# Kernel tuning notes

Hardware: AMD Instinct MI355X
Metric: run time of the kernel (lower is better)

## Reference

```python
import jax, jax.numpy as jnp
import numpy as np

B, SEQ, S, DIM_IN, DIM_K, DIM_V = 4, 2048, 128, 512, 64, 64
L = SEQ + 2 * S
NEG = -1e30  # stand-in for log(0) in the tril mask (finite for stable vjp)


def _layernorm(x, g, b, eps=1e-5):
    m = jnp.mean(x, axis=-1, keepdims=True)
    v = jnp.var(x, axis=-1, keepdims=True)
    return (x - m) / jnp.sqrt(v + eps) * g + b


def setup_inputs() -> dict:
    key = jax.random.key(0)
    ks = jax.random.split(key, 18)
    w = lambda k, shape, s=0.02: (jax.random.normal(k, shape, jnp.float32) * s)
    inp = {
        "x": jax.random.normal(ks[0], (B, L, DIM_IN), jnp.float32),
        "Wq": w(ks[1], (DIM_IN, DIM_K)),
        "Wk": w(ks[2], (DIM_IN, DIM_K)),
        "Wv": w(ks[3], (DIM_IN, DIM_V)),
        "Wq_s": w(ks[4], (DIM_IN, DIM_K)),
        "Wk_s": w(ks[5], (DIM_IN, DIM_K)),
        "Wv_s": w(ks[6], (DIM_IN, DIM_V)),
        "Wq_e": w(ks[7], (DIM_IN, DIM_K)),
        "Wk_e": w(ks[8], (DIM_IN, DIM_K)),
        "Wv_e": w(ks[9], (DIM_IN, DIM_V)),
        "ln_g": jnp.ones((DIM_IN,), jnp.float32),
        "ln_b": jnp.zeros((DIM_IN,), jnp.float32),
        "ln_s_g": jnp.ones((DIM_IN,), jnp.float32),
        "ln_s_b": jnp.zeros((DIM_IN,), jnp.float32),
        "ln_e_g": jnp.ones((DIM_IN,), jnp.float32),
        "ln_e_b": jnp.zeros((DIM_IN,), jnp.float32),
        "cope_emb": jax.random.normal(ks[10], (DIM_K, S), jnp.float32),
        "offset": 0,
    }
    return inp


def reference(x, Wq, Wk, Wv, Wq_s, Wk_s, Wv_s, Wq_e, Wk_e, Wv_e,
              ln_g, ln_b, ln_s_g, ln_s_b, ln_e_g, ln_e_b, cope_emb, offset):
    # extract_state: first/last state_len tokens
    xs, xm, xe = x[:, :S], x[:, S:L - S], x[:, -S:]
    xm = _layernorm(xm, ln_g, ln_b)
    xs = _layernorm(xs, ln_s_g, ln_s_b)
    xe = _layernorm(xe, ln_e_g, ln_e_b)

    q, k, v = xm @ Wq, xm @ Wk, xm @ Wv          # (B, SEQ, dk/dv)
    q_s, k_s, v_s = xs @ Wq_s, xs @ Wk_s, xs @ Wv_s
    q_e, k_e, v_e = xe @ Wq_e, xe @ Wk_e, xe @ Wv_e

    # CoPE bias over the non-state block
    logits = jnp.einsum('bqd,bkd->bqk', q, k)    # (B, SEQ, SEQ)
    gates = jax.nn.sigmoid(logits)
    pos = jnp.flip(jnp.cumsum(jnp.flip(gates, -1), axis=-1), -1)
    pos = jnp.minimum(pos, jnp.float32(S - 1))
    pos_ceil = jnp.ceil(pos).astype(jnp.int32)
    pos_floor = jnp.floor(pos).astype(jnp.int32)
    logits_int = jnp.einsum('bqd,dk->bqk', q, cope_emb)  # (B, SEQ, S)
    logits_c = jnp.take_along_axis(logits_int, pos_ceil, axis=-1)
    logits_f = jnp.take_along_axis(logits_int, pos_floor, axis=-1)
    wfrac = pos - pos_floor.astype(pos.dtype)
    bias = logits_c * wfrac + logits_f * (1.0 - wfrac)   # (B, SEQ, SEQ)

    q_full = jnp.concatenate([q_s, q, q_e], axis=1)      # (B, L, dk)
    k_full = jnp.concatenate([k_s, k, k_e], axis=1)
    v_full = jnp.concatenate([v_s, v, v_e], axis=1)

    # explicit tril log-mask bias with CoPE injected in the middle block
    tri = jnp.tril(jnp.ones((L, L), dtype=bool))
    attn_bias = jnp.where(tri, 0.0, NEG).astype(jnp.float32)
    attn_bias = jnp.broadcast_to(attn_bias, (B, L, L))
    attn_bias = attn_bias.at[:, S:L - S, S:L - S].add(bias)

    scale = 1.0 / jnp.sqrt(jnp.float32(DIM_K))
    scores = jnp.einsum('bqd,bkd->bqk', q_full, k_full) * scale + attn_bias
    att = jax.nn.softmax(scores, axis=-1)
    return jnp.einsum('bqk,bkd->bqd', att, v_full)       # (B, L, dv)
```

## Files before the change

kernel.cpp:

```cpp
#include <hip/hip_runtime.h>
#include <math.h>

#define B_    4
#define SEQ_  2048
#define S_    128
#define L_    2304
#define DIN   512
#define DK    64
#define NEGINF (-1e30f)
#define SCALE 0.125f
#define NCOLS 2176
#define NMID  8192
#define NEDGE 1024
#define LE    2304

typedef _Float16 f16;
typedef __attribute__((ext_vector_type(8))) _Float16 half8;
typedef __attribute__((ext_vector_type(4))) float f32x4;

union U4 { uint4 u; f16 h[8]; };

__global__ __launch_bounds__(256) void k_wsplit(
    const float* __restrict__ Wq,  const float* __restrict__ Wk,  const float* __restrict__ Wv,
    const float* __restrict__ Wqs, const float* __restrict__ Wks, const float* __restrict__ Wvs,
    const float* __restrict__ Wqe, const float* __restrict__ Wke, const float* __restrict__ Wve,
    const float* __restrict__ cope,
    f16* __restrict__ Wsp, f16* __restrict__ copesp)
{
    __shared__ float xs[64 * 68];
    const int kt  = blockIdx.x;
    const int mat = blockIdx.y;
    const int tid = threadIdx.x;

    if (mat == 9) {
        if (kt != 0) return;
        for (int half = 0; half < 2; ++half) {
            #pragma unroll
            for (int i = 0; i < 4; ++i) {
                int g = tid + 256 * i;
                int d = g >> 4, p4 = g & 15;
                *(float4*)(xs + d * 68 + p4 * 4) =
                    *(const float4*)(cope + (size_t)d * 128 + half * 64 + p4 * 4);
            }
            __syncthreads();
            if (tid < 128) {
                int pp = tid & 63, hf = tid >> 6;
                int d0 = hf * 32;
                for (int j = 0; j < 32; ++j) {
                    float v = xs[(d0 + j) * 68 + pp];
                    f16 hi = (f16)v;
                    copesp[(size_t)(half * 64 + pp) * 128 + d0 + j]      = hi;
                    copesp[(size_t)(half * 64 + pp) * 128 + 64 + d0 + j] = (f16)(v - (float)hi);
                }
            }
            __syncthreads();
        }
        return;
    }

    const float* W;
    switch (mat) {
        case 0: W = Wq;  break; case 1: W = Wk;  break; case 2: W = Wv;  break;
        case 3: W = Wqs; break; case 4: W = Wks; break; case 5: W = Wvs; break;
        case 6: W = Wqe; break; case 7: W = Wke; break; default: W = Wve; break;
    }
    const int k0  = kt * 64;
    #pragma unroll
    for (int i = 0; i < 4; ++i) {
        int g = tid + 256 * i;
        int k = g >> 4, c4 = g & 15;
        *(float4*)(xs + k * 68 + c4 * 4) = ((const float4*)W)[(size_t)(k0 + k) * 16 + c4];
    }
    __syncthreads();
    const int col = tid & 63, hf = tid >> 6;
    const int kk0 = hf * 16;
    U4 hi0, hi1, lo0, lo1;
    #pragma unroll
    for (int j = 0; j < 8; ++j) {
        float v0 = xs[(kk0 + j) * 68 + col];
        float v1 = xs[(kk0 + 8 + j) * 68 + col];
        hi0.h[j] = (f16)v0; lo0.h[j] = (f16)(v0 - (float)hi0.h[j]);
        hi1.h[j] = (f16)v1; lo1.h[j] = (f16)(v1 - (float)hi1.h[j]);
    }
    f16* dst = Wsp + (size_t)mat * 65536 + (size_t)col * 1024 + k0 + kk0;
    *(uint4*)(dst)       = hi0.u;
    *(uint4*)(dst + 8)   = hi1.u;
    *(uint4*)(dst + 512) = lo0.u;
    *(uint4*)(dst + 520) = lo1.u;
}

__global__ __launch_bounds__(256) void k_proj(
    const float* __restrict__ x, const f16* __restrict__ Wsp,
    const float* __restrict__ g0, const float* __restrict__ b0,
    const float* __restrict__ gs, const float* __restrict__ bs,
    const float* __restrict__ ge, const float* __restrict__ be,
    f16* __restrict__ qsp, f16* __restrict__ ksp, f16* __restrict__ vhT)
{
    __shared__ f16 As[32 * 136];
    __shared__ f16 Bs[3 * 64 * 136];
    __shared__ float mean_s[32], rstd_s[32];
    const int tid  = threadIdx.x;
    const int row0 = blockIdx.x * 32;
    const int rseq = row0 % L_;
    const int seg  = (rseq < S_) ? 0 : (rseq >= L_ - S_) ? 2 : 1;
    const int mat0 = (seg == 0) ? 3 : (seg == 2) ? 6 : 0;
    const float* gg = (seg == 0) ? gs : (seg == 2) ? ge : g0;
    const float* bb = (seg == 0) ? bs : (seg == 2) ? be : b0;

    {
        const int rr = tid >> 3, qq = tid & 7;
        const float4* xr = (const float4*)(x + (size_t)(row0 + rr) * DIN) + qq * 16;
        float s = 0.f, s2 = 0.f;
        #pragma unroll
        for (int i = 0; i < 16; ++i) {
            float4 v = xr[i];
            s  += v.x + v.y + v.z + v.w;
            s2 += v.x * v.x + v.y * v.y + v.z * v.z + v.w * v.w;
        }
        s  += __shfl_xor(s, 1);  s  += __shfl_xor(s, 2);  s  += __shfl_xor(s, 4);
        s2 += __shfl_xor(s2, 1); s2 += __shfl_xor(s2, 2); s2 += __shfl_xor(s2, 4);
        if (qq == 0) {
            float mean = s * (1.f / DIN);
            mean_s[rr] = mean;
            rstd_s[rr] = rsqrtf(s2 * (1.f / DIN) - mean * mean + 1e-5f);
        }
    }

    const int w = tid >> 6, lane = tid & 63;
    const int cl = lane & 15, quad = lane >> 4;
    const int r0 = 16 * (w >> 1), c0 = 32 * (w & 1);

    f32x4 acc[3][2];
    #pragma unroll
    for (int m = 0; m < 3; ++m)
        #pragma unroll
        for (int j = 0; j < 2; ++j) acc[m][j] = 0.f;

    for (int kc = 0; kc < DIN; kc += 64) {
        __syncthreads();
        {
            int r = tid >> 3, c8 = tid & 7;
            const float* xp = x + (size_t)(row0 + r) * DIN + kc + c8 * 8;
            float4 a0 = *(const float4*)xp;
            float4 a1 = *(const float4*)(xp + 4);
            float4 gA = *(const float4*)(gg + kc + c8 * 8);
            float4 gB = *(const float4*)(gg + kc + c8 * 8 + 4);
            float4 bA = *(const float4*)(bb + kc + c8 * 8);
            float4 bB = *(const float4*)(bb + kc + c8 * 8 + 4);
            float mean = mean_s[r], rstd = rstd_s[r];
            float n[8];
            n[0] = (a0.x - mean) * rstd * gA.x + bA.x;
            n[1] = (a0.y - mean) * rstd * gA.y + bA.y;
            n[2] = (a0.z - mean) * rstd * gA.z + bA.z;
            n[3] = (a0.w - mean) * rstd * gA.w + bA.w;
            n[4] = (a1.x - mean) * rstd * gB.x + bB.x;
            n[5] = (a1.y - mean) * rstd * gB.y + bB.y;
            n[6] = (a1.z - mean) * rstd * gB.z + bB.z;
            n[7] = (a1.w - mean) * rstd * gB.w + bB.w;
            U4 hi, lo;
            #pragma unroll
            for (int j = 0; j < 8; ++j) {
                hi.h[j] = (f16)n[j];
                lo.h[j] = (f16)(n[j] - (float)hi.h[j]);
            }
            *(uint4*)(As + r * 136 + c8 * 8)      = hi.u;
            *(uint4*)(As + r * 136 + 64 + c8 * 8) = lo.u;
        }
        #pragma unroll
        for (int i = 0; i < 6; ++i) {
            int g = tid + 256 * i;
            int mm = g >> 9, rem = g & 511;
            int col = rem >> 3, c8 = rem & 7;
            const f16* src = Wsp + (size_t)(mat0 + mm) * 65536 + (size_t)col * 1024 + kc + c8 * 8;
            f16* dst = Bs + mm * 8704 + col * 136 + c8 * 8;
            *(uint4*)(dst)      = *(const uint4*)(src);
            *(uint4*)(dst + 64) = *(const uint4*)(src + 512);
        }
        __syncthreads();
        #pragma unroll
        for (int h = 0; h < 2; ++h) {
            half8 ah, al;
            {
                const f16* base = As + (r0 + cl) * 136 + h * 32 + quad * 8;
                ah = *(const half8*)(base);
                al = *(const half8*)(base + 64);
            }
            #pragma unroll
            for (int m = 0; m < 3; ++m)
                #pragma unroll
                for (int cs = 0; cs < 2; ++cs) {
                    const f16* base = Bs + m * 8704 + (c0 + 16 * cs + cl) * 136 + h * 32 + quad * 8;
                    half8 bh = *(const half8*)(base);
                    half8 bl = *(const half8*)(base + 64);
                    acc[m][cs] = __builtin_amdgcn_mfma_f32_16x16x32_f16(ah, bh, acc[m][cs], 0, 0, 0);
                    acc[m][cs] = __builtin_amdgcn_mfma_f32_16x16x32_f16(ah, bl, acc[m][cs], 0, 0, 0);
                    acc[m][cs] = __builtin_amdgcn_mfma_f32_16x16x32_f16(al, bh, acc[m][cs], 0, 0, 0);
                }
        }
    }

    const int bI = row0 / L_;
    const int rb = row0 - bI * L_;
    #pragma unroll
    for (int m = 0; m < 3; ++m) {
        f16* sp = (m == 0) ? qsp : ksp;
        #pragma unroll
        for (int cs = 0; cs < 2; ++cs)
            #pragma unroll
            for (int r = 0; r < 4; ++r) {
                int lrow = r0 + quad * 4 + r;
                int col  = c0 + 16 * cs + cl;
                float v  = acc[m][cs][r];
                size_t grow = (size_t)(row0 + lrow);
                if (m < 2) {
                    f16 hv = (f16)v;
                    sp[grow * 128 + col]      = hv;
                    sp[grow * 128 + 64 + col] = (f16)(v - (float)hv);
                } else {
                    vhT[(size_t)(bI * 64 + col) * L_ + rb + lrow] = (f16)v;
                }
            }
    }
}

__global__ __launch_bounds__(512) void k_fmid(
    const f16* __restrict__ qsp, const f16* __restrict__ ksp,
    const f16* __restrict__ vhT, const f16* __restrict__ copesp,
    float* __restrict__ out)
{
    __shared__ f16 Qs[32 * 136];
    __shared__ f16 Ks[128 * 136];
    __shared__ f16 Vt[64 * 136];
    __shared__ float li[32 * 132];
    __shared__ float Tq[4][32], Tm[4][32], Ll[4][32];
    f16* const Ps = Ks + 64 * 136;

    const int tid = threadIdx.x;
    const int blk = blockIdx.x;
    const int b = blk >> 6, strip = blk & 63;
    const int q0 = strip * 32;
    const size_t rowbase = (size_t)b * L_ + S_ + q0;
    const int w = tid >> 6, lane = tid & 63;
    const int cl = lane & 15, quad = lane >> 4;
    const int g = w >> 2, ch = w & 3;
    const int tmax = ((q0 + 31) >> 7) + 1;

    {
        int r = tid >> 4, c = tid & 15;
        *(uint4*)(Qs + r * 136 + c * 8) = *(const uint4*)(qsp + (rowbase + r) * 128 + c * 8);
    }
    __syncthreads();

    {
        f32x4 accli[2];
        accli[0] = 0.f; accli[1] = 0.f;
        #pragma unroll
        for (int h = 0; h < 2; ++h) {
            const f16* abase = Qs + (16 * g + cl) * 136 + h * 32 + quad * 8;
            half8 ah = *(const half8*)(abase);
            half8 al = *(const half8*)(abase + 64);
            #pragma unroll
            for (int cf = 0; cf < 2; ++cf) {
                const f16* bbase = copesp + (size_t)(32 * ch + 16 * cf + cl) * 128 + h * 32 + quad * 8;
                half8 bh = *(const half8*)(bbase);
                half8 bl = *(const half8*)(bbase + 64);
                accli[cf] = __builtin_amdgcn_mfma_f32_16x16x32_f16(ah, bh, accli[cf], 0, 0, 0);
                accli[cf] = __builtin_amdgcn_mfma_f32_16x16x32_f16(ah, bl, accli[cf], 0, 0, 0);
                accli[cf] = __builtin_amdgcn_mfma_f32_16x16x32_f16(al, bh, accli[cf], 0, 0, 0);
            }
        }
        #pragma unroll
        for (int cf = 0; cf < 2; ++cf)
            #pragma unroll
            for (int r = 0; r < 4; ++r)
                li[(16 * g + quad * 4 + r) * 132 + 32 * ch + 16 * cf + cl] = accli[cf][r];
    }

    float R[4]  = {0.f, 0.f, 0.f, 0.f};
    float m_run[4] = {NEGINF, NEGINF, NEGINF, NEGINF};
    float l_run[4] = {0.f, 0.f, 0.f, 0.f};
    f32x4 accO = 0.f;

    for (int t = 16; t >= 0; --t) {
        const bool mid    = (t >= 1);
        const bool causal = (t <= tmax);
        const int kbase   = mid ? (S_ + 128 * (t - 1)) : 0;

        __syncthreads();
        #pragma unroll
        for (int i = 0; i < 4; ++i) {
            int gi = tid + 512 * i;
            int r = gi >> 4, c = gi & 15;
            *(uint4*)(Ks + r * 136 + c * 8) =
                *(const uint4*)(ksp + ((size_t)b * L_ + kbase + r) * 128 + c * 8);
        }
        if (causal) {
            #pragma unroll
            for (int i = 0; i < 2; ++i) {
                int gi = tid + 512 * i;
                int vc = gi >> 4, c = gi & 15;
                *(uint4*)(Vt + vc * 136 + c * 8) =
                    *(const uint4*)(vhT + (size_t)(b * 64 + vc) * L_ + kbase + c * 8);
            }
        }
        __syncthreads();

        f32x4 acc[2];
        acc[0] = 0.f; acc[1] = 0.f;
        #pragma unroll
        for (int h = 0; h < 2; ++h) {
            const f16* abase = Qs + (16 * g + cl) * 136 + h * 32 + quad * 8;
            half8 ah = *(const half8*)(abase);
            half8 al = *(const half8*)(abase + 64);
            #pragma unroll
            for (int cf = 0; cf < 2; ++cf) {
                const f16* bbase = Ks + (32 * ch + 16 * cf + cl) * 136 + h * 32 + quad * 8;
                half8 bh = *(const half8*)(bbase);
                half8 bl = *(const half8*)(bbase + 64);
                acc[cf] = __builtin_amdgcn_mfma_f32_16x16x32_f16(ah, bh, acc[cf], 0, 0, 0);
                acc[cf] = __builtin_amdgcn_mfma_f32_16x16x32_f16(ah, bl, acc[cf], 0, 0, 0);
                acc[cf] = __builtin_amdgcn_mfma_f32_16x16x32_f16(al, bh, acc[cf], 0, 0, 0);
            }
        }

        float sfx[2][4], F1r[4];
        float hq[4], ttot[4];
        if (mid) {
            #pragma unroll
            for (int cf = 0; cf < 2; ++cf)
                #pragma unroll
                for (int r = 0; r < 4; ++r)
                    sfx[cf][r] = 1.f / (1.f + __expf(-acc[cf][r]));
            #pragma unroll
            for (int off = 1; off < 16; off <<= 1) {
                #pragma unroll
                for (int cf = 0; cf < 2; ++cf)
                    #pragma unroll
                    for (int r = 0; r < 4; ++r) {
                        float u = __shfl_down(sfx[cf][r], off, 16);
                        if (cl + off < 16) sfx[cf][r] += u;
                    }
            }
            float F0r[4];
            #pragma unroll
            for (int r = 0; r < 4; ++r) {
                F0r[r] = __shfl(sfx[0][r], 0, 16);
                F1r[r] = __shfl(sfx[1][r], 0, 16);
            }
            if (cl == 0) {
                #pragma unroll
                for (int r = 0; r < 4; ++r)
                    Tq[ch][16 * g + quad * 4 + r] = F0r[r] + F1r[r];
            }
            __syncthreads();
            #pragma unroll
            for (int r = 0; r < 4; ++r) {
                int row = 16 * g + quad * 4 + r;
                float t0 = Tq[0][row], t1 = Tq[1][row], t2 = Tq[2][row], t3 = Tq[3][row];
                ttot[r] = t0 + t1 + t2 + t3;
                hq[r] = (ch == 0) ? (t1 + t2 + t3) : (ch == 1) ? (t2 + t3) : (ch == 2) ? t3 : 0.f;
            }
        }

        if (causal) {
            float p0[2][4];
            float ml[4] = {NEGINF, NEGINF, NEGINF, NEGINF};
            #pragma unroll
            for (int cf = 0; cf < 2; ++cf)
                #pragma unroll
                for (int r = 0; r < 4; ++r) {
                    int row = 16 * g + quad * 4 + r;
                    int q = q0 + row;
                    float sc;
                    if (mid) {
                        int mcol = 128 * (t - 1) + 32 * ch + 16 * cf + cl;
                        float run = sfx[cf][r] + ((cf == 0) ? F1r[r] : 0.f) + hq[r] + R[r];
                        float pos = fminf(run, 127.f);
                        float pfl = floorf(pos);
                        int ic = (int)ceilf(pos), ifl = (int)pfl;
                        float wf = pos - pfl;
                        float bias = li[row * 132 + ic] * wf + li[row * 132 + ifl] * (1.f - wf);
                        sc = (mcol <= q) ? acc[cf][r] * SCALE + bias : NEGINF;
                    } else {
                        sc = acc[cf][r] * SCALE;
                    }
                    p0[cf][r] = sc;
                    ml[r] = fmaxf(ml[r], sc);
                }
            #pragma unroll
            for (int off = 1; off < 16; off <<= 1)
                #pragma unroll
                for (int r = 0; r < 4; ++r)
                    ml[r] = fmaxf(ml[r], __shfl_xor(ml[r], off, 16));
            if (cl == 0) {
                #pragma unroll
                for (int r = 0; r < 4; ++r)
                    Tm[ch][16 * g + quad * 4 + r] = ml[r];
            }
            __syncthreads();
            float rs_[4];
            #pragma unroll
            for (int r = 0; r < 4; ++r) {
                int row = 16 * g + quad * 4 + r;
                float mn = fmaxf(fmaxf(Tm[0][row], Tm[1][row]), fmaxf(Tm[2][row], Tm[3][row]));
                mn = fmaxf(fmaxf(mn, m_run[r]), -1e28f);
                rs_[r] = __expf(m_run[r] - mn);
                m_run[r] = mn;
            }
            float ll[4] = {0.f, 0.f, 0.f, 0.f};
            #pragma unroll
            for (int cf = 0; cf < 2; ++cf)
                #pragma unroll
                for (int r = 0; r < 4; ++r) {
                    int row = 16 * g + quad * 4 + r;
                    float e = __expf(p0[cf][r] - m_run[r]);
                    ll[r] += e;
                    Ps[row * 136 + 32 * ch + 16 * cf + cl] = (f16)e;
                }
            #pragma unroll
            for (int off = 1; off < 16; off <<= 1)
                #pragma unroll
                for (int r = 0; r < 4; ++r)
                    ll[r] += __shfl_xor(ll[r], off, 16);
            if (cl == 0) {
                #pragma unroll
                for (int r = 0; r < 4; ++r)
                    Ll[ch][16 * g + quad * 4 + r] = ll[r];
            }
            #pragma unroll
            for (int r = 0; r < 4; ++r) accO[r] *= rs_[r];
            __syncthreads();
            #pragma unroll
            for (int r = 0; r < 4; ++r) {
                int row = 16 * g + quad * 4 + r;
                l_run[r] = l_run[r] * rs_[r] + Ll[0][row] + Ll[1][row] + Ll[2][row] + Ll[3][row];
            }
            #pragma unroll
            for (int kf = 0; kf < 4; ++kf) {
                half8 a  = *(const half8*)(Ps + (16 * g + cl) * 136 + kf * 32 + quad * 8);
                half8 bv = *(const half8*)(Vt + (16 * ch + cl) * 136 + kf * 32 + quad * 8);
                accO = __builtin_amdgcn_mfma_f32_16x16x32_f16(a, bv, accO, 0, 0, 0);
            }
        }

        if (mid) {
            #pragma unroll
            for (int r = 0; r < 4; ++r) R[r] += ttot[r];
        }
    }

    #pragma unroll
    for (int r = 0; r < 4; ++r) {
        int row = 16 * g + quad * 4 + r;
        int col = 16 * ch + cl;
        out[(rowbase + row) * DK + col] = accO[r] / l_run[r];
    }
}

__global__ __launch_bounds__(256) void k_dotse(
    const f16* __restrict__ qsp, const f16* __restrict__ ksp,
    float* __restrict__ De32)
{
    const int bx = blockIdx.x + 64, by = blockIdx.y;
    int ex = bx - 64;
    int b = ex >> 1;
    int half = ex & 1;
    if (half == 0 && by > 0) return;
    size_t qrow0 = (size_t)b * L_ + (half ? 2176 : 0);
    const int col0 = by * 128;
    const size_t krow0 = (size_t)b * L_ + col0;

    __shared__ f16 Qs[128 * 136];
    __shared__ f16 Ks[128 * 136];
    const int tid = threadIdx.x;

    #pragma unroll
    for (int i = 0; i < 8; ++i) {
        int g = tid + 256 * i;
        int r = g >> 4, c = g & 15;
        *(uint4*)(Qs + r * 136 + c * 8) = *(const uint4*)(qsp + (qrow0 + r) * 128 + c * 8);
        *(uint4*)(Ks + r * 136 + c * 8) = *(const uint4*)(ksp + (krow0 + r) * 128 + c * 8);
    }
    __syncthreads();

    const int w = tid >> 6, lane = tid & 63;
    const int cl = lane & 15, quad = lane >> 4;

    f32x4 acc[2][8];
    #pragma unroll
    for (int i = 0; i < 2; ++i)
        #pragma unroll
        for (int j = 0; j < 8; ++j) acc[i][j] = 0.f;

    #pragma unroll
    for (int h = 0; h < 2; ++h) {
        half8 ah[2], al[2];
        #pragma unroll
        for (int rs = 0; rs < 2; ++rs) {
            const f16* base = Qs + (32 * w + 16 * rs + cl) * 136 + h * 32 + quad * 8;
            ah[rs] = *(const half8*)(base);
            al[rs] = *(const half8*)(base + 64);
        }
        #pragma unroll
        for (int cq = 0; cq < 2; ++cq) {
            half8 bh[4], bl[4];
            #pragma unroll
            for (int cc = 0; cc < 4; ++cc) {
                const f16* base = Ks + (16 * (cq * 4 + cc) + cl) * 136 + h * 32 + quad * 8;
                bh[cc] = *(const half8*)(base);
                bl[cc] = *(const half8*)(base + 64);
            }
            #pragma unroll
            for (int rs = 0; rs < 2; ++rs)
                #pragma unroll
                for (int cc = 0; cc < 4; ++cc) {
                    int c = cq * 4 + cc;
                    acc[rs][c] = __builtin_amdgcn_mfma_f32_16x16x32_f16(ah[rs], bh[cc], acc[rs][c], 0, 0, 0);
                    acc[rs][c] = __builtin_amdgcn_mfma_f32_16x16x32_f16(ah[rs], bl[cc], acc[rs][c], 0, 0, 0);
                    acc[rs][c] = __builtin_amdgcn_mfma_f32_16x16x32_f16(al[rs], bh[cc], acc[rs][c], 0, 0, 0);
                }
        }
    }

    const int er0 = (bx - 64) * 128;
    #pragma unroll
    for (int rs = 0; rs < 2; ++rs)
        #pragma unroll
        for (int c = 0; c < 8; ++c)
            #pragma unroll
            for (int r = 0; r < 4; ++r) {
                int erow = er0 + 32 * w + 16 * rs + quad * 4 + r;
                int n    = col0 + 16 * c + cl;
                De32[(size_t)erow * LE + n] = acc[rs][c][r];
            }
}

__global__ __launch_bounds__(256) void k_scane(
    const float* __restrict__ De32, f16* __restrict__ Dep)
{
    __shared__ float wmax[4], wsum[4];
    const int tid = threadIdx.x;
    const int er  = blockIdx.x;
    const int lane = tid & 63, wid = tid >> 6;
    const int r  = er & 255;
    const int Q  = (r < 128) ? r : (2048 + r);
    const float* Er32 = De32 + (size_t)er * LE;
    f16* Er = Dep + (size_t)er * LE;

    float v[9];
    #pragma unroll
    for (int i = 0; i < 9; ++i) {
        int j = tid + 256 * i;
        float d = Er32[j];
        v[i] = (j <= Q) ? d * SCALE : NEGINF;
    }
    float mx = v[0];
    #pragma unroll
    for (int i = 1; i < 9; ++i) mx = fmaxf(mx, v[i]);
    #pragma unroll
    for (int off = 1; off < 64; off <<= 1) mx = fmaxf(mx, __shfl_xor(mx, off));
    if (lane == 0) wmax[wid] = mx;
    __syncthreads();
    mx = fmaxf(fmaxf(wmax[0], wmax[1]), fmaxf(wmax[2], wmax[3]));

    float lsum = 0.f;
    #pragma unroll
    for (int i = 0; i < 9; ++i) {
        v[i] = __expf(v[i] - mx);
        lsum += v[i];
    }
    #pragma unroll
    for (int off = 1; off < 64; off <<= 1) lsum += __shfl_xor(lsum, off);
    if (lane == 0) wsum[wid] = lsum;
    __syncthreads();
    float inv = 1.f / (wsum[0] + wsum[1] + wsum[2] + wsum[3]);

    #pragma unroll
    for (int i = 0; i < 9; ++i)
        Er[tid + 256 * i] = (f16)(v[i] * inv);
}

__global__ __launch_bounds__(256) void k_pve(
    const f16* __restrict__ Pedge, const f16* __restrict__ vhT,
    float* __restrict__ Oe)
{
    __shared__ f16 Ps[64 * 72];
    __shared__ f16 Vt[64 * 72];
    const int tid = threadIdx.x;
    const int ks  = blockIdx.y;

    int row0 = blockIdx.x * 64;
    int b = row0 >> 8;
    int r0 = row0 & 255;
    const f16* Pb = Pedge;
    const size_t pitch = LE;
    int Qmax = (r0 < 128) ? (r0 + 63) : (2048 + r0 + 63);
    int cmax = Qmax >> 6;
    float* outp = Oe + (size_t)ks * NEDGE * DK;

    const int c_beg = ks * 9;
    int c_end = c_beg + 9;
    if (c_end > 36) c_end = 36;
    if (c_end > cmax + 1) c_end = cmax + 1;

    const int w = tid >> 6, lane = tid & 63;
    const int cl = lane & 15, quad = lane >> 4;
    f32x4 acc[4];
    #pragma unroll
    for (int c = 0; c < 4; ++c) acc[c] = 0.f;

    for (int ch = c_beg; ch < c_end; ++ch) {
        __syncthreads();
        #pragma unroll
        for (int i = 0; i < 2; ++i) {
            int g = tid + 256 * i;
            int r = g >> 3, c = g & 7;
            *(uint4*)(Ps + r * 72 + c * 8) =
                *(const uint4*)(Pb + (size_t)(row0 + r) * pitch + ch * 64 + c * 8);
            *(uint4*)(Vt + r * 72 + c * 8) =
                *(const uint4*)(vhT + (size_t)(b * 64 + r) * L_ + ch * 64 + c * 8);
        }
        __syncthreads();
        #pragma unroll
        for (int h = 0; h < 2; ++h) {
            half8 a = *(const half8*)(Ps + (16 * w + cl) * 72 + h * 32 + quad * 8);
            #pragma unroll
            for (int c = 0; c < 4; ++c) {
                half8 bv = *(const half8*)(Vt + (16 * c + cl) * 72 + h * 32 + quad * 8);
                acc[c] = __builtin_amdgcn_mfma_f32_16x16x32_f16(a, bv, acc[c], 0, 0, 0);
            }
        }
    }
    #pragma unroll
    for (int c = 0; c < 4; ++c)
        #pragma unroll
        for (int r = 0; r < 4; ++r) {
            int mrow = row0 + 16 * w + quad * 4 + r;
            int n    = 16 * c + cl;
            outp[(size_t)mrow * DK + n] = acc[c][r];
        }
}

__global__ __launch_bounds__(256) void k_mergee(
    const float* __restrict__ Oe, float* __restrict__ out)
{
    const int e2 = blockIdx.x * 256 + threadIdx.x;
    const int er = e2 >> 6, c = e2 & 63;
    const int b  = er >> 8, r = er & 255;
    const int gQ = (r < 128) ? r : (2048 + r);
    const int NP = NEDGE * DK;
    float s = Oe[e2] + Oe[e2 + NP] + Oe[e2 + 2 * NP] + Oe[e2 + 3 * NP];
    out[((size_t)b * L_ + gQ) * DK + c] = s;
}

extern "C" void kernel_launch(void* const* d_in, const int* in_sizes, int n_in,
                              void* d_out, int out_size, void* d_ws, size_t ws_size,
                              hipStream_t stream)
{
    const float* x    = (const float*)d_in[0];
    const float* Wq   = (const float*)d_in[1];
    const float* Wk   = (const float*)d_in[2];
    const float* Wv   = (const float*)d_in[3];
    const float* Wqs  = (const float*)d_in[4];
    const float* Wks  = (const float*)d_in[5];
    const float* Wvs  = (const float*)d_in[6];
    const float* Wqe  = (const float*)d_in[7];
    const float* Wke  = (const float*)d_in[8];
    const float* Wve  = (const float*)d_in[9];
    const float* g0   = (const float*)d_in[10];
    const float* b0   = (const float*)d_in[11];
    const float* gs   = (const float*)d_in[12];
    const float* bs   = (const float*)d_in[13];
    const float* ge   = (const float*)d_in[14];
    const float* be   = (const float*)d_in[15];
    const float* cope = (const float*)d_in[16];

    const size_t NR = (size_t)B_ * L_;
    f16*   qsp    = (f16*)d_ws;
    f16*   ksp    = qsp + NR * 128;
    f16*   vhT    = ksp + NR * 128;
    f16*   Wsp    = vhT + NR * 64;
    f16*   copesp = Wsp + (size_t)9 * 65536;
    float* De32   = (float*)(copesp + 16384);
    float* Oe     = De32 + (size_t)NEDGE * LE;
    f16*   Dep    = (f16*)(Oe + (size_t)4 * NEDGE * DK);
    float* out    = (float*)d_out;

    k_wsplit<<<dim3(8, 10), 256, 0, stream>>>(Wq, Wk, Wv, Wqs, Wks, Wvs,
                                              Wqe, Wke, Wve, cope, Wsp, copesp);
    k_proj<<<288, 256, 0, stream>>>(x, Wsp, g0, b0, gs, bs, ge, be,
                                    qsp, ksp, vhT);
    k_dotse<<<dim3(8, 18), 256, 0, stream>>>(qsp, ksp, De32);
    k_fmid<<<256, 512, 0, stream>>>(qsp, ksp, vhT, copesp, out);
    k_scane<<<NEDGE, 256, 0, stream>>>(De32, Dep);
    k_pve<<<dim3(16, 4), 256, 0, stream>>>(Dep, vhT, Oe);
    k_mergee<<<256, 256, 0, stream>>>(Oe, out);
}
```

Before: 227.9 us.

## Split mid-block attention key tiles across waves with split-softmax merge

Restructures k_fmid so each of the 8 waves owns whole 128-key tiles. In a first pass each wave computes per-tile sigmoid gate totals, and a shared suffix sum then gives the CoPE position offsets. Each wave then runs an independent online softmax over its own tiles, loading Q into registers and K/V directly from global memory instead of staging them in LDS. Per-wave max, sum and output partials are merged at the end through a shared-memory tree reduction. This removes the per-tile block-wide barriers of the sequential loop, at the cost of computing QK twice for mid tiles, more register pressure (launch bounds set to 1 block) and uneven work across waves due to the causal tmax.

Measured after the change: 247.4 us. +8.6%, slower.

```diff
diff --git a/kernel.cpp b/kernel.cpp
--- a/kernel.cpp
+++ b/kernel.cpp
@@ -9,7 +9,6 @@
 #define DK    64
 #define NEGINF (-1e30f)
 #define SCALE 0.125f
-#define NCOLS 2176
 #define NMID  8192
 #define NEDGE 1024
 #define LE    2304
@@ -223,52 +222,52 @@
     }
 }
 
-__global__ __launch_bounds__(512) void k_fmid(
+__global__ __launch_bounds__(512, 1) void k_fmid(
     const f16* __restrict__ qsp, const f16* __restrict__ ksp,
     const f16* __restrict__ vhT, const f16* __restrict__ copesp,
     float* __restrict__ out)
 {
-    __shared__ f16 Qs[32 * 136];
-    __shared__ f16 Ks[128 * 136];
-    __shared__ f16 Vt[64 * 136];
     __shared__ float li[32 * 132];
-    __shared__ float Tq[4][32], Tm[4][32], Ll[4][32];
-    f16* const Ps = Ks + 64 * 136;
+    __shared__ float Tt[16][32];
+    __shared__ float Rr[16][32];
+    __shared__ float Mw[8][32], Lw[8][32];
+    __shared__ f16   Ps[8][32 * 34];
+    __shared__ float obuf[4][32 * 66];
 
     const int tid = threadIdx.x;
+    const int w = tid >> 6, lane = tid & 63;
+    const int cl = lane & 15, quad = lane >> 4;
     const int blk = blockIdx.x;
     const int b = blk >> 6, strip = blk & 63;
     const int q0 = strip * 32;
     const size_t rowbase = (size_t)b * L_ + S_ + q0;
-    const int w = tid >> 6, lane = tid & 63;
-    const int cl = lane & 15, quad = lane >> 4;
-    const int g = w >> 2, ch = w & 3;
     const int tmax = ((q0 + 31) >> 7) + 1;
 
+    half8 qh[2][2], ql[2][2];
+    #pragma unroll
+    for (int rs = 0; rs < 2; ++rs)
+        #pragma unroll
+        for (int h = 0; h < 2; ++h) {
+            const f16* qp = qsp + (rowbase + 16 * rs + cl) * 128 + h * 32 + quad * 8;
+            qh[rs][h] = *(const half8*)qp;
+            ql[rs][h] = *(const half8*)(qp + 64);
+        }
+
     {
-        int r = tid >> 4, c = tid & 15;
-        *(uint4*)(Qs + r * 136 + c * 8) = *(const uint4*)(qsp + (rowbase + r) * 128 + c * 8);
-    }
-    __syncthreads();
-
-    {
+        const int g = w >> 2, ch = w & 3;
         f32x4 accli[2];
         accli[0] = 0.f; accli[1] = 0.f;
         #pragma unroll
-        for (int h = 0; h < 2; ++h) {
-            const f16* abase = Qs + (16 * g + cl) * 136 + h * 32 + quad * 8;
-            half8 ah = *(const half8*)(abase);
-            half8 al = *(const half8*)(abase + 64);
+        for (int h = 0; h < 2; ++h)
             #pragma unroll
             for (int cf = 0; cf < 2; ++cf) {
                 const f16* bbase = copesp + (size_t)(32 * ch + 16 * cf + cl) * 128 + h * 32 + quad * 8;
-                half8 bh = *(const half8*)(bbase);
+                half8 bh = *(const half8*)bbase;
                 half8 bl = *(const half8*)(bbase + 64);
-                accli[cf] = __builtin_amdgcn_mfma_f32_16x16x32_f16(ah, bh, accli[cf], 0, 0, 0);
-                accli[cf] = __builtin_amdgcn_mfma_f32_16x16x32_f16(ah, bl, accli[cf], 0, 0, 0);
-                accli[cf] = __builtin_amdgcn_mfma_f32_16x16x32_f16(al, bh, accli[cf], 0, 0, 0);
-            }
-        }
+                accli[cf] = __builtin_amdgcn_mfma_f32_16x16x32_f16(qh[g][h], bh, accli[cf], 0, 0, 0);
+                accli[cf] = __builtin_amdgcn_mfma_f32_16x16x32_f16(qh[g][h], bl, accli[cf], 0, 0, 0);
+                accli[cf] = __builtin_amdgcn_mfma_f32_16x16x32_f16(ql[g][h], bh, accli[cf], 0, 0, 0);
+            }
         #pragma unroll
         for (int cf = 0; cf < 2; ++cf)
             #pragma unroll
@@ -276,184 +275,319 @@
                 li[(16 * g + quad * 4 + r) * 132 + 32 * ch + 16 * cf + cl] = accli[cf][r];
     }
 
-    float R[4]  = {0.f, 0.f, 0.f, 0.f};
-    float m_run[4] = {NEGINF, NEGINF, NEGINF, NEGINF};
-    float l_run[4] = {0.f, 0.f, 0.f, 0.f};
-    f32x4 accO = 0.f;
-
-    for (int t = 16; t >= 0; --t) {
-        const bool mid    = (t >= 1);
-        const bool causal = (t <= tmax);
-        const int kbase   = mid ? (S_ + 128 * (t - 1)) : 0;
-
-        __syncthreads();
-        #pragma unroll
-        for (int i = 0; i < 4; ++i) {
-            int gi = tid + 512 * i;
-            int r = gi >> 4, c = gi & 15;
-            *(uint4*)(Ks + r * 136 + c * 8) =
-                *(const uint4*)(ksp + ((size_t)b * L_ + kbase + r) * 128 + c * 8);
-        }
-        if (causal) {
-            #pragma unroll
-            for (int i = 0; i < 2; ++i) {
-                int gi = tid + 512 * i;
-                int vc = gi >> 4, c = gi & 15;
-                *(uint4*)(Vt + vc * 136 + c * 8) =
-                    *(const uint4*)(vhT + (size_t)(b * 64 + vc) * L_ + kbase + c * 8);
-            }
-        }
-        __syncthreads();
-
-        f32x4 acc[2];
-        acc[0] = 0.f; acc[1] = 0.f;
-        #pragma unroll
-        for (int h = 0; h < 2; ++h) {
-            const f16* abase = Qs + (16 * g + cl) * 136 + h * 32 + quad * 8;
-            half8 ah = *(const half8*)(abase);
-            half8 al = *(const half8*)(abase + 64);
-            #pragma unroll
-            for (int cf = 0; cf < 2; ++cf) {
-                const f16* bbase = Ks + (32 * ch + 16 * cf + cl) * 136 + h * 32 + quad * 8;
-                half8 bh = *(const half8*)(bbase);
-                half8 bl = *(const half8*)(bbase + 64);
-                acc[cf] = __builtin_amdgcn_mfma_f32_16x16x32_f16(ah, bh, acc[cf], 0, 0, 0);
-                acc[cf] = __builtin_amdgcn_mfma_f32_16x16x32_f16(ah, bl, acc[cf], 0, 0, 0);
-                acc[cf] = __builtin_amdgcn_mfma_f32_16x16x32_f16(al, bh, acc[cf], 0, 0, 0);
-            }
-        }
-
-        float sfx[2][4], F1r[4];
-        float hq[4], ttot[4];
+    #pragma unroll
+    for (int pp = 0; pp < 2; ++pp) {
+        const int t = 1 + w + 8 * pp;
+        const size_t rowK = (size_t)b * L_ + S_ + 128 * (t - 1);
+        f32x4 acc[2][8];
+        #pragma unroll
+        for (int i = 0; i < 2; ++i)
+            #pragma unroll
+            for (int j = 0; j < 8; ++j) acc[i][j] = 0.f;
+        #pragma unroll
+        for (int h = 0; h < 2; ++h)
+            #pragma unroll
+            for (int c = 0; c < 8; ++c) {
+                const f16* kp = ksp + (rowK + 16 * c + cl) * 128 + h * 32 + quad * 8;
+                half8 bh = *(const half8*)kp;
+                half8 bl = *(const half8*)(kp + 64);
+                #pragma unroll
+                for (int rs = 0; rs < 2; ++rs) {
+                    acc[rs][c] = __builtin_amdgcn_mfma_f32_16x16x32_f16(qh[rs][h], bh, acc[rs][c], 0, 0, 0);
+                    acc[rs][c] = __builtin_amdgcn_mfma_f32_16x16x32_f16(qh[rs][h], bl, acc[rs][c], 0, 0, 0);
+                    acc[rs][c] = __builtin_amdgcn_mfma_f32_16x16x32_f16(ql[rs][h], bh, acc[rs][c], 0, 0, 0);
+                }
+            }
+        #pragma unroll
+        for (int rs = 0; rs < 2; ++rs)
+            #pragma unroll
+            for (int r = 0; r < 4; ++r) {
+                float s = 0.f;
+                #pragma unroll
+                for (int c = 0; c < 8; ++c)
+                    s += 1.f / (1.f + __expf(-acc[rs][c][r]));
+                s += __shfl_xor(s, 1, 16); s += __shfl_xor(s, 2, 16);
+                s += __shfl_xor(s, 4, 16); s += __shfl_xor(s, 8, 16);
+                if (cl == 0) Tt[t - 1][16 * rs + quad * 4 + r] = s;
+            }
+    }
+    __syncthreads();
+
+    {
+        int row = tid & 31, t = (tid >> 5) + 1;
+        float s = 0.f;
+        for (int u = t; u < 16; ++u) s += Tt[u][row];
+        Rr[t - 1][row] = s;
+    }
+    __syncthreads();
+
+    float m_w[2][4], l_w[2][4], tot1[2][4];
+    f32x4 accO[2][4];
+    #pragma unroll
+    for (int rs = 0; rs < 2; ++rs)
+        #pragma unroll
+        for (int r = 0; r < 4; ++r) { m_w[rs][r] = NEGINF; l_w[rs][r] = 0.f; tot1[rs][r] = 0.f; }
+    #pragma unroll
+    for (int rs = 0; rs < 2; ++rs)
+        #pragma unroll
+        for (int c = 0; c < 4; ++c) accO[rs][c] = 0.f;
+
+    for (int t = w; t <= tmax; t += 8) {
+        const bool mid = (t >= 1);
+        const int vbase = mid ? (S_ + 128 * (t - 1)) : 0;
+        const size_t rowK = (size_t)b * L_ + vbase;
+        float Rbase[2][4];
         if (mid) {
             #pragma unroll
-            for (int cf = 0; cf < 2; ++cf)
+            for (int rs = 0; rs < 2; ++rs)
                 #pragma unroll
                 for (int r = 0; r < 4; ++r)
-                    sfx[cf][r] = 1.f / (1.f + __expf(-acc[cf][r]));
-            #pragma unroll
-            for (int off = 1; off < 16; off <<= 1) {
-                #pragma unroll
-                for (int cf = 0; cf < 2; ++cf)
+                    Rbase[rs][r] = Rr[t - 1][16 * rs + quad * 4 + r];
+        }
+        #pragma unroll
+        for (int hx = 1; hx >= 0; --hx) {
+            const int cb = 4 * hx;
+            f32x4 acc[2][4];
+            #pragma unroll
+            for (int i = 0; i < 2; ++i)
+                #pragma unroll
+                for (int j = 0; j < 4; ++j) acc[i][j] = 0.f;
+            #pragma unroll
+            for (int h = 0; h < 2; ++h)
+                #pragma unroll
+                for (int c = 0; c < 4; ++c) {
+                    const f16* kp = ksp + (rowK + 16 * (cb + c) + cl) * 128 + h * 32 + quad * 8;
+                    half8 bh = *(const half8*)kp;
+                    half8 bl = *(const half8*)(kp + 64);
+                    #pragma unroll
+                    for (int rs = 0; rs < 2; ++rs) {
+                        acc[rs][c] = __builtin_amdgcn_mfma_f32_16x16x32_f16(qh[rs][h], bh, acc[rs][c], 0, 0, 0);
+                        acc[rs][c] = __builtin_amdgcn_mfma_f32_16x16x32_f16(qh[rs][h], bl, acc[rs][c], 0, 0, 0);
+                        acc[rs][c] = __builtin_amdgcn_mfma_f32_16x16x32_f16(ql[rs][h], bh, acc[rs][c], 0, 0, 0);
+                    }
+                }
+
+            float sfx[2][4][4];
+            if (mid) {
+                #pragma unroll
+                for (int rs = 0; rs < 2; ++rs)
+                    #pragma unroll
+                    for (int c = 0; c < 4; ++c)
+                        #pragma unroll
+                        for (int r = 0; r < 4; ++r)
+                            sfx[rs][c][r] = 1.f / (1.f + __expf(-acc[rs][c][r]));
+                #pragma unroll
+                for (int off = 1; off < 16; off <<= 1)
+                    #pragma unroll
+                    for (int rs = 0; rs < 2; ++rs)
+                        #pragma unroll
+                        for (int c = 0; c < 4; ++c)
+                            #pragma unroll
+                            for (int r = 0; r < 4; ++r) {
+                                float u = __shfl_down(sfx[rs][c][r], off, 16);
+                                if (cl + off < 16) sfx[rs][c][r] += u;
+                            }
+                #pragma unroll
+                for (int rs = 0; rs < 2; ++rs)
                     #pragma unroll
                     for (int r = 0; r < 4; ++r) {
-                        float u = __shfl_down(sfx[cf][r], off, 16);
-                        if (cl + off < 16) sfx[cf][r] += u;
+                        float tc0 = __shfl(sfx[rs][0][r], 0, 16);
+                        float tc1 = __shfl(sfx[rs][1][r], 0, 16);
+                        float tc2 = __shfl(sfx[rs][2][r], 0, 16);
+                        float tc3 = __shfl(sfx[rs][3][r], 0, 16);
+                        float run = 0.f;
+                        sfx[rs][3][r] += run; run += tc3;
+                        sfx[rs][2][r] += run; run += tc2;
+                        sfx[rs][1][r] += run; run += tc1;
+                        sfx[rs][0][r] += run; run += tc0;
+                        if (hx == 1) tot1[rs][r] = run;
                     }
             }
-            float F0r[4];
+
+            #pragma unroll
+            for (int rs = 0; rs < 2; ++rs)
+                #pragma unroll
+                for (int c = 0; c < 4; ++c)
+                    #pragma unroll
+                    for (int r = 0; r < 4; ++r) {
+                        int row = 16 * rs + quad * 4 + r;
+                        float v = acc[rs][c][r] * SCALE;
+                        if (mid) {
+                            float pos = sfx[rs][c][r] + Rbase[rs][r] + ((hx == 0) ? tot1[rs][r] : 0.f);
+                            pos = fminf(pos, 127.f);
+                            float pfl = floorf(pos);
+                            int ic = (int)ceilf(pos), ifl = (int)pfl;
+                            float wf = pos - pfl;
+                            v += li[row * 132 + ic] * wf + li[row * 132 + ifl] * (1.f - wf);
+                            int mcol = 128 * (t - 1) + 16 * (cb + c) + cl;
+                            if (mcol > q0 + row) v = NEGINF;
+                        }
+                        acc[rs][c][r] = v;
+                    }
+
+            float scf[2][4];
+            #pragma unroll
+            for (int rs = 0; rs < 2; ++rs)
+                #pragma unroll
+                for (int r = 0; r < 4; ++r) {
+                    float ml = fmaxf(fmaxf(acc[rs][0][r], acc[rs][1][r]),
+                                     fmaxf(acc[rs][2][r], acc[rs][3][r]));
+                    ml = fmaxf(ml, __shfl_xor(ml, 1, 16));
+                    ml = fmaxf(ml, __shfl_xor(ml, 2, 16));
+                    ml = fmaxf(ml, __shfl_xor(ml, 4, 16));
+                    ml = fmaxf(ml, __shfl_xor(ml, 8, 16));
+                    float mn = fmaxf(fmaxf(m_w[rs][r], ml), -1e28f);
+                    scf[rs][r] = __expf(m_w[rs][r] - mn);
+                    m_w[rs][r] = mn;
+                }
+            #pragma unroll
+            for (int rs = 0; rs < 2; ++rs)
+                #pragma unroll
+                for (int c = 0; c < 4; ++c)
+                    #pragma unroll
+                    for (int r = 0; r < 4; ++r)
+                        accO[rs][c][r] *= scf[rs][r];
+
+            float lsum[2][4];
+            #pragma unroll
+            for (int rs = 0; rs < 2; ++rs)
+                #pragma unroll
+                for (int r = 0; r < 4; ++r) lsum[rs][r] = 0.f;
+            #pragma unroll
+            for (int rs = 0; rs < 2; ++rs)
+                #pragma unroll
+                for (int c = 0; c < 4; ++c)
+                    #pragma unroll
+                    for (int r = 0; r < 4; ++r) {
+                        float e = __expf(acc[rs][c][r] - m_w[rs][r]);
+                        acc[rs][c][r] = e;
+                        lsum[rs][r] += e;
+                    }
+            #pragma unroll
+            for (int rs = 0; rs < 2; ++rs)
+                #pragma unroll
+                for (int r = 0; r < 4; ++r) {
+                    float s = lsum[rs][r];
+                    s += __shfl_xor(s, 1, 16); s += __shfl_xor(s, 2, 16);
+                    s += __shfl_xor(s, 4, 16); s += __shfl_xor(s, 8, 16);
+                    l_w[rs][r] = l_w[rs][r] * scf[rs][r] + s;
+                }
+
+            #pragma unroll
+            for (int kfl = 0; kfl < 2; ++kfl) {
+                #pragma unroll
+                for (int rs = 0; rs < 2; ++rs)
+                    #pragma unroll
+                    for (int cw = 0; cw < 2; ++cw)
+                        #pragma unroll
+                        for (int r = 0; r < 4; ++r)
+                            Ps[w][(16 * rs + quad * 4 + r) * 34 + 16 * cw + cl] =
+                                (f16)acc[rs][2 * kfl + cw][r];
+                half8 pa[2];
+                #pragma unroll
+                for (int rs2 = 0; rs2 < 2; ++rs2)
+                    pa[rs2] = *(const half8*)&Ps[w][(16 * rs2 + cl) * 34 + quad * 8];
+                const int kf = 2 * hx + kfl;
+                #pragma unroll
+                for (int c2 = 0; c2 < 4; ++c2) {
+                    const f16* vp = vhT + (size_t)(b * 64 + 16 * c2 + cl) * L_ + vbase + kf * 32 + quad * 8;
+                    half8 bv = *(const half8*)vp;
+                    #pragma unroll
+                    for (int rs2 = 0; rs2 < 2; ++rs2)
+                        accO[rs2][c2] = __builtin_amdgcn_mfma_f32_16x16x32_f16(pa[rs2], bv, accO[rs2][c2], 0, 0, 0);
+                }
+            }
+        }
+    }
+
+    if (cl == 0) {
+        #pragma unroll
+        for (int rs = 0; rs < 2; ++rs)
             #pragma unroll
             for (int r = 0; r < 4; ++r) {
-                F0r[r] = __shfl(sfx[0][r], 0, 16);
-                F1r[r] = __shfl(sfx[1][r], 0, 16);
-            }
-            if (cl == 0) {
+                Mw[w][16 * rs + quad * 4 + r] = m_w[rs][r];
+                Lw[w][16 * rs + quad * 4 + r] = l_w[rs][r];
+            }
+    }
+    __syncthreads();
+
+    float lg[2][4];
+    #pragma unroll
+    for (int rs = 0; rs < 2; ++rs)
+        #pragma unroll
+        for (int r = 0; r < 4; ++r) {
+            int row = 16 * rs + quad * 4 + r;
+            float m = Mw[0][row];
+            #pragma unroll
+            for (int i = 1; i < 8; ++i) m = fmaxf(m, Mw[i][row]);
+            float s = 0.f;
+            #pragma unroll
+            for (int i = 0; i < 8; ++i) s += Lw[i][row] * __expf(Mw[i][row] - m);
+            lg[rs][r] = s;
+            float scf = __expf(m_w[rs][r] - m);
+            #pragma unroll
+            for (int c = 0; c < 4; ++c) accO[rs][c][r] *= scf;
+        }
+
+    if (w >= 4) {
+        #pragma unroll
+        for (int rs = 0; rs < 2; ++rs)
+            #pragma unroll
+            for (int c = 0; c < 4; ++c)
                 #pragma unroll
                 for (int r = 0; r < 4; ++r)
-                    Tq[ch][16 * g + quad * 4 + r] = F0r[r] + F1r[r];
-            }
-            __syncthreads();
-            #pragma unroll
-            for (int r = 0; r < 4; ++r) {
-                int row = 16 * g + quad * 4 + r;
-                float t0 = Tq[0][row], t1 = Tq[1][row], t2 = Tq[2][row], t3 = Tq[3][row];
-                ttot[r] = t0 + t1 + t2 + t3;
-                hq[r] = (ch == 0) ? (t1 + t2 + t3) : (ch == 1) ? (t2 + t3) : (ch == 2) ? t3 : 0.f;
-            }
-        }
-
-        if (causal) {
-            float p0[2][4];
-            float ml[4] = {NEGINF, NEGINF, NEGINF, NEGINF};
-            #pragma unroll
-            for (int cf = 0; cf < 2; ++cf)
+                    obuf[w - 4][(16 * rs + quad * 4 + r) * 66 + 16 * c + cl] = accO[rs][c][r];
+    }
+    __syncthreads();
+    if (w < 4) {
+        #pragma unroll
+        for (int rs = 0; rs < 2; ++rs)
+            #pragma unroll
+            for (int c = 0; c < 4; ++c)
+                #pragma unroll
+                for (int r = 0; r < 4; ++r)
+                    accO[rs][c][r] += obuf[w][(16 * rs + quad * 4 + r) * 66 + 16 * c + cl];
+        if (w >= 2) {
+            #pragma unroll
+            for (int rs = 0; rs < 2; ++rs)
+                #pragma unroll
+                for (int c = 0; c < 4; ++c)
+                    #pragma unroll
+                    for (int r = 0; r < 4; ++r)
+                        obuf[w][(16 * rs + quad * 4 + r) * 66 + 16 * c + cl] = accO[rs][c][r];
+        }
+    }
+    __syncthreads();
+    if (w < 2) {
+        #pragma unroll
+        for (int rs = 0; rs < 2; ++rs)
+            #pragma unroll
+            for (int c = 0; c < 4; ++c)
+                #pragma unroll
+                for (int r = 0; r < 4; ++r)
+                    accO[rs][c][r] += obuf[w + 2][(16 * rs + quad * 4 + r) * 66 + 16 * c + cl];
+        if (w == 1) {
+            #pragma unroll
+            for (int rs = 0; rs < 2; ++rs)
+                #pragma unroll
+                for (int c = 0; c < 4; ++c)
+                    #pragma unroll
+                    for (int r = 0; r < 4; ++r)
+                        obuf[1][(16 * rs + quad * 4 + r) * 66 + 16 * c + cl] = accO[rs][c][r];
+        }
+    }
+    __syncthreads();
+    if (w == 0) {
+        #pragma unroll
+        for (int rs = 0; rs < 2; ++rs)
+            #pragma unroll
+            for (int c = 0; c < 4; ++c)
                 #pragma unroll
                 for (int r = 0; r < 4; ++r) {
-                    int row = 16 * g + quad * 4 + r;
-                    int q = q0 + row;
-                    float sc;
-                    if (mid) {
-                        int mcol = 128 * (t - 1) + 32 * ch + 16 * cf + cl;
-                        float run = sfx[cf][r] + ((cf == 0) ? F1r[r] : 0.f) + hq[r] + R[r];
-                        float pos = fminf(run, 127.f);
-                        float pfl = floorf(pos);
-                        int ic = (int)ceilf(pos), ifl = (int)pfl;
-                        float wf = pos - pfl;
-                        float bias = li[row * 132 + ic] * wf + li[row * 132 + ifl] * (1.f - wf);
-                        sc = (mcol <= q) ? acc[cf][r] * SCALE + bias : NEGINF;
-                    } else {
-                        sc = acc[cf][r] * SCALE;
-                    }
-                    p0[cf][r] = sc;
-                    ml[r] = fmaxf(ml[r], sc);
-                }
-            #pragma unroll
-            for (int off = 1; off < 16; off <<= 1)
-                #pragma unroll
-                for (int r = 0; r < 4; ++r)
-                    ml[r] = fmaxf(ml[r], __shfl_xor(ml[r], off, 16));
-            if (cl == 0) {
-                #pragma unroll
-                for (int r = 0; r < 4; ++r)
-                    Tm[ch][16 * g + quad * 4 + r] = ml[r];
-            }
-            __syncthreads();
-            float rs_[4];
-            #pragma unroll
-            for (int r = 0; r < 4; ++r) {
-                int row = 16 * g + quad * 4 + r;
-                float mn = fmaxf(fmaxf(Tm[0][row], Tm[1][row]), fmaxf(Tm[2][row], Tm[3][row]));
-                mn = fmaxf(fmaxf(mn, m_run[r]), -1e28f);
-                rs_[r] = __expf(m_run[r] - mn);
-                m_run[r] = mn;
-            }
-            float ll[4] = {0.f, 0.f, 0.f, 0.f};
-            #pragma unroll
-            for (int cf = 0; cf < 2; ++cf)
-                #pragma unroll
-                for (int r = 0; r < 4; ++r) {
-                    int row = 16 * g + quad * 4 + r;
-                    float e = __expf(p0[cf][r] - m_run[r]);
-                    ll[r] += e;
-                    Ps[row * 136 + 32 * ch + 16 * cf + cl] = (f16)e;
-                }
-            #pragma unroll
-            for (int off = 1; off < 16; off <<= 1)
-                #pragma unroll
-                for (int r = 0; r < 4; ++r)
-                    ll[r] += __shfl_xor(ll[r], off, 16);
-            if (cl == 0) {
-                #pragma unroll
-                for (int r = 0; r < 4; ++r)
-                    Ll[ch][16 * g + quad * 4 + r] = ll[r];
-            }
-            #pragma unroll
-            for (int r = 0; r < 4; ++r) accO[r] *= rs_[r];
-            __syncthreads();
-            #pragma unroll
-            for (int r = 0; r < 4; ++r) {
-                int row = 16 * g + quad * 4 + r;
-                l_run[r] = l_run[r] * rs_[r] + Ll[0][row] + Ll[1][row] + Ll[2][row] + Ll[3][row];
-            }
-            #pragma unroll
-            for (int kf = 0; kf < 4; ++kf) {
-                half8 a  = *(const half8*)(Ps + (16 * g + cl) * 136 + kf * 32 + quad * 8);
-                half8 bv = *(const half8*)(Vt + (16 * ch + cl) * 136 + kf * 32 + quad * 8);
-                accO = __builtin_amdgcn_mfma_f32_16x16x32_f16(a, bv, accO, 0, 0, 0);
-            }
-        }
-
-        if (mid) {
-            #pragma unroll
-            for (int r = 0; r < 4; ++r) R[r] += ttot[r];
-        }
-    }
-
-    #pragma unroll
-    for (int r = 0; r < 4; ++r) {
-        int row = 16 * g + quad * 4 + r;
-        int col = 16 * ch + cl;
-        out[(rowbase + row) * DK + col] = accO[r] / l_run[r];
+                    float v = accO[rs][c][r] + obuf[1][(16 * rs + quad * 4 + r) * 66 + 16 * c + cl];
+                    int row = 16 * rs + quad * 4 + r;
+                    out[(rowbase + row) * DK + 16 * c + cl] = v / lg[rs][r];
+                }
     }
 }
 
```
